# Performance work log

Hardware: AMD Instinct MI355X
Metric: run time of the kernel (lower is better)

## Reference

```python
import jax, jax.numpy as jnp
import numpy as np

# dims: S spaces, B batch, T tokens, D = dense_dim = concept_dim, K codebook size
S, B, T, D, K = 8, 8, 2048, 64, 512
BN_EPS = 1e-3  # keras BatchNormalization default


def setup_inputs() -> dict:
    key = jax.random.key(0)
    k0, k1, k2 = jax.random.split(key, 3)
    x = jax.random.normal(k0, (B, T, D), jnp.float32)
    W = jax.random.normal(k1, (S, D, D), jnp.float32) * 0.1   # per-space Dense kernels
    b = jnp.zeros((S, D), jnp.float32)                         # per-space Dense biases
    gamma = jnp.ones((S, D), jnp.float32)                      # BN scale
    beta = jnp.zeros((S, D), jnp.float32)                      # BN shift
    bn_mean = jnp.zeros((S, D), jnp.float32)                   # BN moving mean
    bn_var = jnp.ones((S, D), jnp.float32)                     # BN moving var
    E = jax.random.normal(k2, (S, K, D), jnp.float32)          # per-space codebooks
    return dict(x=x, W=W, b=b, gamma=gamma, beta=beta,
                bn_mean=bn_mean, bn_var=bn_var, E=E)


def reference(x, W, b, gamma, beta, bn_mean, bn_var, E):
    # per-space projection: Dense -> BatchNorm (inference) -> softmax gate
    proj = jnp.einsum('btd,sde->sbte', x, W) + b[:, None, None, :]          # [S,B,T,D]
    inv = jax.lax.rsqrt(bn_var + BN_EPS)
    bn = gamma[:, None, None, :] * (proj - bn_mean[:, None, None, :]) * inv[:, None, None, :] \
         + beta[:, None, None, :]
    att = jax.nn.softmax(bn, axis=-1)
    z = x[None] * att                                                       # z_e_att, [S,B,T,D]

    # squared euclidean distance to each code; argmin(norm) == argmin(dist^2)
    d2 = (jnp.sum(z * z, axis=-1, keepdims=True)
          - 2.0 * jnp.einsum('sbtc,skc->sbtk', z, E)
          + jnp.sum(E * E, axis=-1)[:, None, None, :])                      # [S,B,T,K]
    z_k = jnp.argmin(d2, axis=-1)                                           # [S,B,T] int

    # gather nearest codes per space, then add_n over spaces (set_att != 0)
    z_q_s = E[jnp.arange(S)[:, None, None], z_k]                            # [S,B,T,D]
    z_q = jnp.sum(z_q_s, axis=0)                                            # [B,T,D]
    z_e = jnp.sum(z, axis=0)                                                # [B,T,D]
    z_k = z_k.astype(jnp.int64) if z_k.dtype != jnp.int64 else z_k          # tf.argmin -> int64
    return z_q, z_e, z_k
```

## Files before the change

kernel.cpp:

```cpp
#include <hip/hip_runtime.h>
#include <cfloat>
#include <cmath>

#define SN 8
#define DN 64
#define KN 512
#define NN 16384
#define CK 64
#define REPAIR_THR 2e-3f
#define GAP_IK 8u
#define MAXFLAG 32768

#define WS_CNT 0
#define WS_SCL 16
#define WS_OFF (16 + SN*DN)
#define WS_E2  (WS_OFF + SN*DN)
#define WS_ENT (WS_E2 + SN*KN)
#define WS_WTH (WS_ENT + MAXFLAG)
#define WS_WTL (WS_WTH + SN*64*32)
#define WS_EH  (WS_WTL + SN*64*32)
#define WS_EL  (WS_EH + SN*KN*32)
#define WS_ZP  (WS_EL + SN*KN*32)
#define WS_E2S (WS_ZP + SN*NN*DN)
#define WS_END (WS_E2S + SN*KN)

#define LDS_ZH 0
#define LDS_ZL 8192
#define LDS_E0 16384
#define LDS_TOTAL 49152

#define FB_LDS_R2    17408
#define FB_LDS_TAIL  33792
#define FB_LDS_TOTAL 34816

typedef __attribute__((ext_vector_type(8))) short bf16x8;
typedef __attribute__((ext_vector_type(4))) short s16x4;
typedef __attribute__((ext_vector_type(4))) float f32x4;

__device__ inline short bf_hi(float f, float& rem) {
    unsigned u = __float_as_uint(f);
    unsigned r = (u + 0x7fffu + ((u >> 16) & 1u)) & 0xffff0000u;
    rem = f - __uint_as_float(r);
    return (short)(r >> 16);
}
__device__ inline short bf_rn(float f) {
    unsigned u = __float_as_uint(f);
    return (short)((u + 0x7fffu + ((u >> 16) & 1u)) >> 16);
}
__device__ inline void cvt4(float a, float b, float c, float d, s16x4& h, s16x4& l) {
    float r0, r1, r2, r3;
    h.x = bf_hi(a, r0); h.y = bf_hi(b, r1); h.z = bf_hi(c, r2); h.w = bf_hi(d, r3);
    l.x = bf_rn(r0); l.y = bf_rn(r1); l.z = bf_rn(r2); l.w = bf_rn(r3);
}

union U8 { bf16x8 v; s16x4 q[2]; };

__global__ void prep_all_kernel(const float* __restrict__ b, const float* __restrict__ gamma,
                                const float* __restrict__ beta, const float* __restrict__ bmean,
                                const float* __restrict__ bvar, const float* __restrict__ W,
                                const float* __restrict__ E, float* __restrict__ ws) {
    __shared__ float wt[64][65];
    const int blk = blockIdx.x, tid = threadIdx.x;
    if (blk < 256) {
        int idx = blk * 256 + tid;
        int sk = idx >> 4, c4 = idx & 15;
        int k = sk & (KN - 1);
        float4 g = ((const float4*)E)[(size_t)sk * 16 + c4];
        s16x4 h4, l4;
        cvt4(g.x, g.y, g.z, g.w, h4, l4);
        size_t off = ((size_t)sk * 128 + c4 * 8) ^ ((k & 7) << 4);
        *(s16x4*)((char*)(ws + WS_EH) + off) = h4;
        *(s16x4*)((char*)(ws + WS_EL) + off) = l4;
    } else if (blk < 264) {
        int s = blk - 256;
        #pragma unroll
        for (int r = 0; r < 4; ++r) {
            int i = r * 256 + tid;
            float4 g = ((const float4*)W)[(size_t)s * 1024 + i];
            int d = i >> 4, c4 = i & 15;
            wt[d][c4 * 4 + 0] = g.x; wt[d][c4 * 4 + 1] = g.y;
            wt[d][c4 * 4 + 2] = g.z; wt[d][c4 * 4 + 3] = g.w;
        }
        __syncthreads();
        #pragma unroll
        for (int r = 0; r < 4; ++r) {
            int j = r * 256 + tid;
            int e = j >> 4, c4 = j & 15;
            s16x4 h4, l4;
            cvt4(wt[c4 * 4 + 0][e], wt[c4 * 4 + 1][e], wt[c4 * 4 + 2][e], wt[c4 * 4 + 3][e], h4, l4);
            size_t off = (size_t)(s * 64 + e) * 128 + c4 * 8;
            *(s16x4*)((char*)(ws + WS_WTH) + off) = h4;
            *(s16x4*)((char*)(ws + WS_WTL) + off) = l4;
        }
    } else {
        int t2 = (blk - 264) * 256 + tid;
        if (t2 < SN * KN) {
            const float* er = E + (size_t)t2 * DN;
            double a = 0.0;
            for (int d = 0; d < DN; ++d) { double v = (double)er[d]; a = fma(v, v, a); }
            ws[WS_E2 + t2]  = (float)a;
            ws[WS_E2S + t2] = (float)(a * 4096.0);
        }
        int u = t2 - SN * KN;
        if (u >= 0 && u < SN * DN) {
            double inv = 1.0 / sqrt((double)bvar[u] + 0.001);
            double sc  = (double)gamma[u] * inv;
            ws[WS_SCL + u] = (float)sc;
            ws[WS_OFF + u] = (float)(((double)b[u] - (double)bmean[u]) * sc + (double)beta[u]);
        }
    }
}

__global__ void prep_kernel(const float* __restrict__ b, const float* __restrict__ gamma,
                            const float* __restrict__ beta, const float* __restrict__ bmean,
                            const float* __restrict__ bvar, const float* __restrict__ E,
                            float* __restrict__ ws) {
    int tid = blockIdx.x * 256 + threadIdx.x;
    if (tid < SN * KN) {
        const float* er = E + (size_t)tid * DN;
        double a = 0.0;
        for (int d = 0; d < DN; ++d) { double v = (double)er[d]; a = fma(v, v, a); }
        ws[WS_E2 + tid] = (float)a;
    }
    int u = tid - SN * KN;
    if (u >= 0 && u < SN * DN) {
        double inv = 1.0 / sqrt((double)bvar[u] + 0.001);
        double sc  = (double)gamma[u] * inv;
        ws[WS_SCL + u] = (float)sc;
        ws[WS_OFF + u] = (float)(((double)b[u] - (double)bmean[u]) * sc + (double)beta[u]);
    }
}

__launch_bounds__(256, 3)
__global__ void main_kernel(const float* __restrict__ x, float* __restrict__ ws,
                            float* __restrict__ out, int entcap) {
    extern __shared__ char smraw[];
    const int tid = threadIdx.x;
    const int s  = blockIdx.y;
    const int n0 = blockIdx.x * 64;
    const int lane = tid & 63;
    const int w    = tid >> 6;
    const int cc   = lane & 15;
    const int kq   = lane >> 4;
    const int arow = w * 16 + cc;
    const int axor = (arow & 7) << 4;

    const char* eimg_h = (const char*)(ws + WS_EH) + (size_t)s * KN * 128;
    const char* eimg_l = (const char*)(ws + WS_EL) + (size_t)s * KN * 128;

    float4 pf0 = *(const float4*)(eimg_h + tid * 16);
    float4 pf1 = *(const float4*)(eimg_h + 4096 + tid * 16);
    float4 pf2 = *(const float4*)(eimg_l + tid * 16);
    float4 pf3 = *(const float4*)(eimg_l + 4096 + tid * 16);

    U8 xah[2], xal[2];
    #pragma unroll
    for (int ks = 0; ks < 2; ++ks) {
        const float* xr = x + (size_t)(n0 + arow) * DN + ks * 32 + kq * 8;
        float4 a = *(const float4*)xr;
        float4 b2 = *(const float4*)(xr + 4);
        s16x4 h0, l0, h1, l1;
        cvt4(a.x, a.y, a.z, a.w, h0, l0);
        cvt4(b2.x, b2.y, b2.z, b2.w, h1, l1);
        xah[ks].q[0] = h0; xah[ks].q[1] = h1;
        xal[ks].q[0] = l0; xal[ks].q[1] = l1;
    }

    const char* wimg_h = (const char*)(ws + WS_WTH) + (size_t)s * 64 * 128;
    const char* wimg_l = (const char*)(ws + WS_WTL) + (size_t)s * 64 * 128;
    f32x4 pa[4];
    #pragma unroll
    for (int nt = 0; nt < 4; ++nt) pa[nt] = (f32x4){0.f, 0.f, 0.f, 0.f};
    #pragma unroll
    for (int ks = 0; ks < 2; ++ks) {
        #pragma unroll
        for (int nt = 0; nt < 4; ++nt) {
            int brow = nt * 16 + cc;
            bf16x8 bh = *(const bf16x8*)(wimg_h + brow * 128 + ks * 64 + kq * 16);
            bf16x8 bl = *(const bf16x8*)(wimg_l + brow * 128 + ks * 64 + kq * 16);
            pa[nt] = __builtin_amdgcn_mfma_f32_16x16x32_bf16(xah[ks].v, bh, pa[nt], 0, 0, 0);
            pa[nt] = __builtin_amdgcn_mfma_f32_16x16x32_bf16(xah[ks].v, bl, pa[nt], 0, 0, 0);
            pa[nt] = __builtin_amdgcn_mfma_f32_16x16x32_bf16(xal[ks].v, bh, pa[nt], 0, 0, 0);
        }
    }

    float sclv[4], oflv[4];
    #pragma unroll
    for (int nt = 0; nt < 4; ++nt) {
        sclv[nt] = ws[WS_SCL + s * 64 + nt * 16 + cc];
        oflv[nt] = ws[WS_OFF + s * 64 + nt * 16 + cc];
    }
    float zzq[4];
    #pragma unroll
    for (int r = 0; r < 4; ++r) {
        int t = w * 16 + kq * 4 + r;
        float v0 = fmaf(pa[0][r], sclv[0], oflv[0]);
        float v1 = fmaf(pa[1][r], sclv[1], oflv[1]);
        float v2 = fmaf(pa[2][r], sclv[2], oflv[2]);
        float v3 = fmaf(pa[3][r], sclv[3], oflv[3]);
        float mx = fmaxf(fmaxf(v0, v1), fmaxf(v2, v3));
        mx = fmaxf(mx, __shfl_xor(mx, 1)); mx = fmaxf(mx, __shfl_xor(mx, 2));
        mx = fmaxf(mx, __shfl_xor(mx, 4)); mx = fmaxf(mx, __shfl_xor(mx, 8));
        float e0 = __expf(v0 - mx), e1 = __expf(v1 - mx);
        float e2v = __expf(v2 - mx), e3 = __expf(v3 - mx);
        float sm = e0 + e1 + e2v + e3;
        sm += __shfl_xor(sm, 1); sm += __shfl_xor(sm, 2);
        sm += __shfl_xor(sm, 4); sm += __shfl_xor(sm, 8);
        float inv = 1.0f / sm;
        float att[4] = { e0 * inv, e1 * inv, e2v * inv, e3 * inv };
        float zz = 0.f;
        int txor = (t & 7) << 4;
        #pragma unroll
        for (int nt = 0; nt < 4; ++nt) {
            int e = nt * 16 + cc;
            float xv = x[(size_t)(n0 + t) * DN + e];
            float z = xv * att[nt];
            zz += z * z;
            float rem; short zh = bf_hi(z, rem); short zl = bf_rn(rem);
            int zoff = (t * 128 + e * 2) ^ txor;
            *(short*)(smraw + LDS_ZH + zoff) = zh;
            *(short*)(smraw + LDS_ZL + zoff) = zl;
            ws[WS_ZP + ((size_t)s * NN + n0 + t) * DN + e] = z;
        }
        zz += __shfl_xor(zz, 1); zz += __shfl_xor(zz, 2);
        zz += __shfl_xor(zz, 4); zz += __shfl_xor(zz, 8);
        zzq[r] = (zz + 16.f) * 4096.f;
    }

    bf16x8 zah[2], zal[2];
    #pragma unroll
    for (int ks = 0; ks < 2; ++ks) {
        int aoff = (arow * 128 + kq * 16 + ks * 64) ^ axor;
        zah[ks] = *(const bf16x8*)(smraw + LDS_ZH + aoff);
        zal[ks] = *(const bf16x8*)(smraw + LDS_ZL + aoff);
    }

    unsigned m1[4], m2[4];
    #pragma unroll
    for (int r = 0; r < 4; ++r) { m1[r] = 0xFFFFFFFFu; m2[r] = 0xFFFFFFFFu; }

    int p = 0;
    #pragma unroll 1
    for (int c = 0; c < KN / CK; ++c) {
        char* ebuf = smraw + LDS_E0 + p * 16384;
        *(float4*)(ebuf + tid * 16) = pf0;
        *(float4*)(ebuf + 4096 + tid * 16) = pf1;
        *(float4*)(ebuf + 8192 + tid * 16) = pf2;
        *(float4*)(ebuf + 12288 + tid * 16) = pf3;
        __syncthreads();

        int kk = c * CK;
        if (c < KN / CK - 1) {
            const char* nbh = eimg_h + (size_t)(kk + CK) * 128;
            const char* nbl = eimg_l + (size_t)(kk + CK) * 128;
            pf0 = *(const float4*)(nbh + tid * 16);
            pf1 = *(const float4*)(nbh + 4096 + tid * 16);
            pf2 = *(const float4*)(nbl + tid * 16);
            pf3 = *(const float4*)(nbl + 4096 + tid * 16);
        }
        float e2v[4];
        #pragma unroll
        for (int nt = 0; nt < 4; ++nt) e2v[nt] = ws[WS_E2S + s * KN + kk + nt * 16 + cc];

        f32x4 acc[4];
        #pragma unroll
        for (int nt = 0; nt < 4; ++nt) acc[nt] = (f32x4){0.f, 0.f, 0.f, 0.f};
        #pragma unroll
        for (int ks = 0; ks < 2; ++ks) {
            #pragma unroll
            for (int nt = 0; nt < 4; ++nt) {
                int brow = nt * 16 + cc;
                int boff = (brow * 128 + kq * 16 + ks * 64) ^ ((brow & 7) << 4);
                bf16x8 bh = *(const bf16x8*)(ebuf + boff);
                bf16x8 bl = *(const bf16x8*)(ebuf + 8192 + boff);
                acc[nt] = __builtin_amdgcn_mfma_f32_16x16x32_bf16(zah[ks], bh, acc[nt], 0, 0, 0);
                acc[nt] = __builtin_amdgcn_mfma_f32_16x16x32_bf16(zah[ks], bl, acc[nt], 0, 0, 0);
                acc[nt] = __builtin_amdgcn_mfma_f32_16x16x32_bf16(zal[ks], bh, acc[nt], 0, 0, 0);
            }
        }
        #pragma unroll
        for (int nt = 0; nt < 4; ++nt) {
            unsigned kx = (unsigned)(kk + nt * 16 + cc);
            #pragma unroll
            for (int r = 0; r < 4; ++r) {
                float cell = fmaf(-8192.f, acc[nt][r], zzq[r] + e2v[nt]);
                unsigned key = (((unsigned)cell) << 9) | kx;
                m2[r] = min(m2[r], max(m1[r], key));
                m1[r] = min(m1[r], key);
            }
        }
        p ^= 1;
    }

    #pragma unroll
    for (int mask = 1; mask <= 8; mask <<= 1) {
        #pragma unroll
        for (int r = 0; r < 4; ++r) {
            unsigned o1 = (unsigned)__shfl_xor((int)m1[r], mask);
            unsigned o2 = (unsigned)__shfl_xor((int)m2[r], mask);
            unsigned hi = max(m1[r], o1);
            m1[r] = min(m1[r], o1);
            m2[r] = min(min(m2[r], o2), hi);
        }
    }
    #pragma unroll
    for (int r = 0; r < 4; ++r) {
        int n = n0 + w * 16 + kq * 4 + r;
        if (cc == 0) {
            int k1 = (int)(m1[r] & 511u);
            out[2 * NN * DN + s * NN + n] = (float)k1;
            if ((m2[r] >> 9) - (m1[r] >> 9) <= GAP_IK) {
                int idx = atomicAdd((int*)ws, 1);
                if (idx < entcap) ((int*)ws)[WS_ENT + idx] = (s << 14) | n;
            }
        }
    }
}

__launch_bounds__(256, 4)
__global__ void main_fb_kernel(const float* __restrict__ x, const float* __restrict__ W,
                               const float* __restrict__ E, float* __restrict__ ws,
                               float* __restrict__ out, int entcap) {
    extern __shared__ char smraw[];
    float4* xs4 = (float4*)smraw;
    float4* ws4 = (float4*)(smraw + FB_LDS_R2);
    char* ehb = smraw;
    char* elb = smraw + 8192;
    char* zhb = smraw + FB_LDS_R2;
    char* zlb = smraw + FB_LDS_R2 + 8192;
    float* tailf = (float*)(smraw + FB_LDS_TAIL);
    float* e2s = tailf; float* scl = tailf + 64; float* ofl = tailf + 128; float* zzs = tailf + 192;

    const int tid = threadIdx.x;
    const int tg = tid >> 4, lg = tid & 15;
    const int s  = blockIdx.y;
    const int n0 = blockIdx.x * 64;
    const float4* xg4 = (const float4*)x;
    const float4* Wg4 = (const float4*)W;
    const float4* Eg4 = (const float4*)E;

    #pragma unroll
    for (int r = 0; r < 4; ++r) {
        int i = r * 256 + tid;
        xs4[(i >> 4) * 17 + (i & 15)] = xg4[n0 * 16 + i];
        ws4[i] = Wg4[s * 1024 + i];
    }
    if (tid < 64) { scl[tid] = ws[WS_SCL + s * 64 + tid]; ofl[tid] = ws[WS_OFF + s * 64 + tid]; }
    __syncthreads();

    float pa[4][4];
    #pragma unroll
    for (int ti = 0; ti < 4; ++ti)
        #pragma unroll
        for (int j = 0; j < 4; ++j) pa[ti][j] = 0.f;
    #pragma unroll 4
    for (int c = 0; c < 16; ++c) {
        float4 xv[4], wv[4];
        #pragma unroll
        for (int ti = 0; ti < 4; ++ti) xv[ti] = xs4[(tg * 4 + ti) * 17 + c];
        #pragma unroll
        for (int dd = 0; dd < 4; ++dd) wv[dd] = ws4[(c * 4 + dd) * 16 + lg];
        #pragma unroll
        for (int ti = 0; ti < 4; ++ti) {
            float a0 = pa[ti][0], a1 = pa[ti][1], a2 = pa[ti][2], a3 = pa[ti][3];
            a0 = fmaf(xv[ti].x, wv[0].x, a0); a0 = fmaf(xv[ti].y, wv[1].x, a0);
            a0 = fmaf(xv[ti].z, wv[2].x, a0); a0 = fmaf(xv[ti].w, wv[3].x, a0);
            a1 = fmaf(xv[ti].x, wv[0].y, a1); a1 = fmaf(xv[ti].y, wv[1].y, a1);
            a1 = fmaf(xv[ti].z, wv[2].y, a1); a1 = fmaf(xv[ti].w, wv[3].y, a1);
            a2 = fmaf(xv[ti].x, wv[0].z, a2); a2 = fmaf(xv[ti].y, wv[1].z, a2);
            a2 = fmaf(xv[ti].z, wv[2].z, a2); a2 = fmaf(xv[ti].w, wv[3].z, a2);
            a3 = fmaf(xv[ti].x, wv[0].w, a3); a3 = fmaf(xv[ti].y, wv[1].w, a3);
            a3 = fmaf(xv[ti].z, wv[2].w, a3); a3 = fmaf(xv[ti].w, wv[3].w, a3);
            pa[ti][0] = a0; pa[ti][1] = a1; pa[ti][2] = a2; pa[ti][3] = a3;
        }
    }
    __syncthreads();

    {
        float s0 = scl[lg * 4 + 0], s1 = scl[lg * 4 + 1], s2 = scl[lg * 4 + 2], s3 = scl[lg * 4 + 3];
        float o0 = ofl[lg * 4 + 0], o1 = ofl[lg * 4 + 1], o2 = ofl[lg * 4 + 2], o3 = ofl[lg * 4 + 3];
        #pragma unroll
        for (int ti = 0; ti < 4; ++ti) {
            int t = tg * 4 + ti;
            float v0 = fmaf(pa[ti][0], s0, o0);
            float v1 = fmaf(pa[ti][1], s1, o1);
            float v2 = fmaf(pa[ti][2], s2, o2);
            float v3 = fmaf(pa[ti][3], s3, o3);
            float mx = fmaxf(fmaxf(v0, v1), fmaxf(v2, v3));
            mx = fmaxf(mx, __shfl_xor(mx, 1)); mx = fmaxf(mx, __shfl_xor(mx, 2));
            mx = fmaxf(mx, __shfl_xor(mx, 4)); mx = fmaxf(mx, __shfl_xor(mx, 8));
            float e0 = expf(v0 - mx), e1 = expf(v1 - mx), e2v = expf(v2 - mx), e3 = expf(v3 - mx);
            float sm = e0 + e1 + e2v + e3;
            sm += __shfl_xor(sm, 1); sm += __shfl_xor(sm, 2);
            sm += __shfl_xor(sm, 4); sm += __shfl_xor(sm, 8);
            float inv = 1.0f / sm;
            float4 xv = xs4[t * 17 + lg];
            float z0 = xv.x * (e0 * inv), z1 = xv.y * (e1 * inv);
            float z2 = xv.z * (e2v * inv), z3 = xv.w * (e3 * inv);
            float zz = z0 * z0 + z1 * z1 + z2 * z2 + z3 * z3;
            zz += __shfl_xor(zz, 1); zz += __shfl_xor(zz, 2);
            zz += __shfl_xor(zz, 4); zz += __shfl_xor(zz, 8);
            if (lg == 0) zzs[t] = zz;
            s16x4 h4, l4;
            cvt4(z0, z1, z2, z3, h4, l4);
            int zoff = (t * 128 + lg * 8) ^ ((t & 7) << 4);
            *(s16x4*)(zhb + zoff) = h4;
            *(s16x4*)(zlb + zoff) = l4;
            float* pz = out + NN * DN + (size_t)(n0 + t) * DN + lg * 4;
            atomicAdd(pz + 0, z0); atomicAdd(pz + 1, z1);
            atomicAdd(pz + 2, z2); atomicAdd(pz + 3, z3);
        }
    }
    __syncthreads();

    const int lane = tid & 63;
    const int w    = tid >> 6;
    const int arow = w * 16 + (lane & 15);
    const int kg16 = (lane >> 4) * 16;
    const int axor = (arow & 7) << 4;
    const int abase = arow * 128 + kg16;

    float zzv[4];
    #pragma unroll
    for (int r = 0; r < 4; ++r) zzv[r] = zzs[w * 16 + (lane >> 4) * 4 + r];

    float m1[4], m2[4]; int k1[4];
    #pragma unroll
    for (int r = 0; r < 4; ++r) { m1[r] = FLT_MAX; m2[r] = FLT_MAX; k1[r] = 0x7fffffff; }

    for (int kk = 0; kk < KN; kk += CK) {
        __syncthreads();
        #pragma unroll
        for (int r = 0; r < 4; ++r) {
            int i = r * 256 + tid;
            float4 g = Eg4[(s * KN + kk) * 16 + i];
            int row = i >> 4, c4 = i & 15;
            s16x4 h4, l4;
            cvt4(g.x, g.y, g.z, g.w, h4, l4);
            int off = (row * 128 + c4 * 8) ^ ((row & 7) << 4);
            *(s16x4*)(ehb + off) = h4;
            *(s16x4*)(elb + off) = l4;
        }
        if (tid < 64) e2s[tid] = ws[WS_E2 + s * KN + kk + tid];
        __syncthreads();

        f32x4 acc[4];
        #pragma unroll
        for (int nt = 0; nt < 4; ++nt) acc[nt] = (f32x4){0.f, 0.f, 0.f, 0.f};
        #pragma unroll
        for (int ks = 0; ks < 2; ++ks) {
            int aoff = (abase + ks * 64) ^ axor;
            bf16x8 ah = *(const bf16x8*)(zhb + aoff);
            bf16x8 al = *(const bf16x8*)(zlb + aoff);
            #pragma unroll
            for (int nt = 0; nt < 4; ++nt) {
                int brow = nt * 16 + (lane & 15);
                int boff = (brow * 128 + kg16 + ks * 64) ^ ((brow & 7) << 4);
                bf16x8 bh = *(const bf16x8*)(ehb + boff);
                bf16x8 bl = *(const bf16x8*)(elb + boff);
                acc[nt] = __builtin_amdgcn_mfma_f32_16x16x32_bf16(ah, bh, acc[nt], 0, 0, 0);
                acc[nt] = __builtin_amdgcn_mfma_f32_16x16x32_bf16(ah, bl, acc[nt], 0, 0, 0);
                acc[nt] = __builtin_amdgcn_mfma_f32_16x16x32_bf16(al, bh, acc[nt], 0, 0, 0);
            }
        }
        #pragma unroll
        for (int nt = 0; nt < 4; ++nt) {
            float e2v = e2s[nt * 16 + (lane & 15)];
            int kx = kk + nt * 16 + (lane & 15);
            #pragma unroll
            for (int r = 0; r < 4; ++r) {
                float d2 = fmaf(-2.0f, acc[nt][r], zzv[r]) + e2v;
                if (d2 < m1[r]) { m2[r] = m1[r]; m1[r] = d2; k1[r] = kx; }
                else if (d2 < m2[r]) { m2[r] = d2; }
            }
        }
    }

    #pragma unroll
    for (int mask = 1; mask <= 8; mask <<= 1) {
        #pragma unroll
        for (int r = 0; r < 4; ++r) {
            float om1 = __shfl_xor(m1[r], mask);
            int   ok1 = __shfl_xor(k1[r], mask);
            float om2 = __shfl_xor(m2[r], mask);
            bool better = (om1 < m1[r]) || (om1 == m1[r] && ok1 < k1[r]);
            float nm2 = better ? fminf(m1[r], om2) : fminf(om1, m2[r]);
            if (better) { m1[r] = om1; k1[r] = ok1; }
            m2[r] = nm2;
        }
    }
    #pragma unroll
    for (int r = 0; r < 4; ++r) {
        int t = w * 16 + (lane >> 4) * 4 + r;
        int n = n0 + t;
        if ((lane & 15) == 0) {
            out[2 * NN * DN + s * NN + n] = (float)k1[r];
            if (m2[r] - m1[r] < REPAIR_THR) {
                int idx = atomicAdd((int*)ws, 1);
                if (idx < entcap) ((int*)ws)[WS_ENT + idx] = (s << 14) | n;
            }
        }
        int kb = __shfl(k1[r], lane & 48);
        float4 eg = Eg4[(s * KN + kb) * 16 + (lane & 15)];
        float* q = out + (size_t)n * DN + (lane & 15) * 4;
        atomicAdd(q + 0, eg.x); atomicAdd(q + 1, eg.y);
        atomicAdd(q + 2, eg.z); atomicAdd(q + 3, eg.w);
    }
}

__global__ void reduce_kernel(const float* __restrict__ E, const float* __restrict__ ws,
                              float* __restrict__ out) {
    int idx = blockIdx.x * 256 + threadIdx.x;
    int n = idx >> 4, c = idx & 15;
    const float4* zp4 = (const float4*)(ws + WS_ZP);
    float4 ze = make_float4(0.f, 0.f, 0.f, 0.f);
    #pragma unroll
    for (int s = 0; s < SN; ++s) {
        float4 v = zp4[((size_t)s * NN + n) * 16 + c];
        ze.x += v.x; ze.y += v.y; ze.z += v.z; ze.w += v.w;
    }
    ((float4*)out)[NN * 16 + (size_t)n * 16 + c] = ze;

    float4 zq = make_float4(0.f, 0.f, 0.f, 0.f);
    #pragma unroll
    for (int s = 0; s < SN; ++s) {
        int k = (int)(out[2 * NN * DN + s * NN + n] + 0.5f);
        float4 e = ((const float4*)E)[((size_t)s * KN + k) * 16 + c];
        zq.x += e.x; zq.y += e.y; zq.z += e.z; zq.w += e.w;
    }
    ((float4*)out)[(size_t)n * 16 + c] = zq;
}

__global__ void repair_kernel(const float* __restrict__ x, const float* __restrict__ W,
                              const float* __restrict__ b, const float* __restrict__ gamma,
                              const float* __restrict__ beta, const float* __restrict__ bmean,
                              const float* __restrict__ bvar, const float* __restrict__ E,
                              float* __restrict__ ws, float* __restrict__ out, int entcap) {
    __shared__ double zd[64];
    __shared__ double red[256];
    __shared__ int redk[256];
    __shared__ double zzsh;
    __shared__ int shk[2];
    int cnt = ((int*)ws)[0]; if (cnt > entcap) cnt = entcap;
    const int tid = threadIdx.x;
    for (int idx = blockIdx.x; idx < cnt; idx += gridDim.x) {
        int code = ((int*)ws)[WS_ENT + idx];
        int s = code >> 14, n = code & (NN - 1);
        int e = tid & 63, q = tid >> 6;
        const float* xrow = x + (size_t)n * 64;
        double p0 = 0.0, p1 = 0.0, p2 = 0.0, p3 = 0.0;
        for (int d = q * 16; d < q * 16 + 16; d += 4) {
            p0 = fma((double)xrow[d],     (double)W[((size_t)s * 64 + d) * 64 + e],     p0);
            p1 = fma((double)xrow[d + 1], (double)W[((size_t)s * 64 + d + 1) * 64 + e], p1);
            p2 = fma((double)xrow[d + 2], (double)W[((size_t)s * 64 + d + 2) * 64 + e], p2);
            p3 = fma((double)xrow[d + 3], (double)W[((size_t)s * 64 + d + 3) * 64 + e], p3);
        }
        red[tid] = (p0 + p1) + (p2 + p3);
        __syncthreads();
        if (tid < 64) {
            double proj = (red[tid] + red[tid + 64]) + (red[tid + 128] + red[tid + 192]);
            double inv = 1.0 / sqrt((double)bvar[s * 64 + e] + 0.001);
            double bn = (double)gamma[s * 64 + e] * ((proj + (double)b[s * 64 + e]) - (double)bmean[s * 64 + e]) * inv
                      + (double)beta[s * 64 + e];
            double m = bn;
            #pragma unroll
            for (int mask = 1; mask <= 32; mask <<= 1) m = fmax(m, __shfl_xor(m, mask));
            double ex = exp(bn - m);
            double sm = ex;
            #pragma unroll
            for (int mask = 1; mask <= 32; mask <<= 1) sm += __shfl_xor(sm, mask);
            double z = (double)xrow[e] * (ex / sm);
            zd[e] = z;
            double zz = z * z;
            #pragma unroll
            for (int mask = 1; mask <= 32; mask <<= 1) zz += __shfl_xor(zz, mask);
            if (tid == 0) zzsh = zz;
        }
        __syncthreads();
        double bv = DBL_MAX; int bk = 1 << 30;
        for (int k = tid; k < KN; k += 256) {
            const float* er = E + ((size_t)s * KN + k) * 64;
            double d0 = 0.0, d1 = 0.0, d2a = 0.0, d3 = 0.0;
            double f0 = 0.0, f1 = 0.0, f2 = 0.0, f3 = 0.0;
            for (int d = 0; d < 64; d += 4) {
                double e0 = (double)er[d], e1 = (double)er[d + 1];
                double e2d = (double)er[d + 2], e3d = (double)er[d + 3];
                d0 = fma(zd[d], e0, d0);     d1 = fma(zd[d + 1], e1, d1);
                d2a = fma(zd[d + 2], e2d, d2a); d3 = fma(zd[d + 3], e3d, d3);
                f0 = fma(e0, e0, f0); f1 = fma(e1, e1, f1);
                f2 = fma(e2d, e2d, f2); f3 = fma(e3d, e3d, f3);
            }
            double dot = (d0 + d1) + (d2a + d3);
            double e2t = (f0 + f1) + (f2 + f3);
            double d2v = (zzsh - 2.0 * dot) + e2t;
            if (d2v < bv) { bv = d2v; bk = k; }
        }
        #pragma unroll
        for (int mask = 1; mask <= 32; mask <<= 1) {
            double ov = __shfl_xor(bv, mask);
            int   ok = __shfl_xor(bk, mask);
            if (ov < bv || (ov == bv && ok < bk)) { bv = ov; bk = ok; }
        }
        if ((tid & 63) == 0) { red[tid >> 6] = bv; redk[tid >> 6] = bk; }
        __syncthreads();
        if (tid == 0) {
            double m = red[0]; int mk = redk[0];
            for (int i = 1; i < 4; ++i)
                if (red[i] < m || (red[i] == m && redk[i] < mk)) { m = red[i]; mk = redk[i]; }
            int kold = (int)(out[2 * NN * 64 + s * NN + n] + 0.5f);
            shk[0] = mk; shk[1] = kold;
            out[2 * NN * 64 + s * NN + n] = (float)mk;
        }
        __syncthreads();
        int mk = shk[0], kold = shk[1];
        if (mk != kold && tid < 64)
            atomicAdd(out + n * 64 + tid, E[((size_t)s * KN + mk) * 64 + tid] - E[((size_t)s * KN + kold) * 64 + tid]);
        __syncthreads();
    }
}

extern "C" void kernel_launch(void* const* d_in, const int* in_sizes, int n_in,
                              void* d_out, int out_size, void* d_ws, size_t ws_size,
                              hipStream_t stream) {
    const float* x     = (const float*)d_in[0];
    const float* W     = (const float*)d_in[1];
    const float* b     = (const float*)d_in[2];
    const float* gamma = (const float*)d_in[3];
    const float* beta  = (const float*)d_in[4];
    const float* bmean = (const float*)d_in[5];
    const float* bvar  = (const float*)d_in[6];
    const float* E     = (const float*)d_in[7];
    float* out = (float*)d_out;
    float* ws  = (float*)d_ws;

    bool staged = ws_size >= (size_t)WS_END * 4;

    long avail = (long)(ws_size / 4) - WS_ENT - 16;
    if (avail < 0) avail = 0;
    int entcap = (int)(avail > MAXFLAG ? MAXFLAG : avail);
    if (staged) entcap = MAXFLAG;

    hipMemsetAsync(d_ws, 0, 64, stream);
    dim3 grid(256, 8);
    if (staged) {
        prep_all_kernel<<<282, 256, 0, stream>>>(b, gamma, beta, bmean, bvar, W, E, ws);
        main_kernel<<<grid, 256, LDS_TOTAL, stream>>>(x, ws, out, entcap);
        reduce_kernel<<<1024, 256, 0, stream>>>(E, ws, out);
    } else {
        prep_kernel<<<18, 256, 0, stream>>>(b, gamma, beta, bmean, bvar, E, ws);
        hipMemsetAsync(d_out, 0, (size_t)(2 * NN * DN) * sizeof(float), stream);
        main_fb_kernel<<<grid, 256, FB_LDS_TOTAL, stream>>>(x, W, E, ws, out, entcap);
    }
    repair_kernel<<<2048, 256, 0, stream>>>(x, W, b, gamma, beta, bmean, bvar, E, ws, out, entcap);
}
```

Baseline: 153.0 us.

## Double block tile to 128 rows, restage codebook pipeline, coalesce z spill

Main kernel blocks grow from 256 to 512 threads and cover 128 tokens each, so every codebook chunk staged in LDS is reused by twice as many rows. The codebook prefetch is restructured so each chunk is written to the alternate buffer after the compute, giving one barrier per chunk. The per-element z spill to workspace is replaced by a coalesced float4 write reconstructed from the bf16 hi/lo pair held in LDS. The workspace memset is folded into the prep kernel, and the repair gap threshold is halved. Risks: the reconstructed z is not bit-identical to the fp32 value, and the larger LDS footprint and block size can lower occupancy.

```diff
diff --git a/kernel.cpp b/kernel.cpp
--- a/kernel.cpp
+++ b/kernel.cpp
@@ -8,7 +8,7 @@
 #define NN 16384
 #define CK 64
 #define REPAIR_THR 2e-3f
-#define GAP_IK 8u
+#define GAP_IK 4u
 #define MAXFLAG 32768
 
 #define WS_CNT 0
@@ -25,9 +25,9 @@
 #define WS_END (WS_E2S + SN*KN)
 
 #define LDS_ZH 0
-#define LDS_ZL 8192
-#define LDS_E0 16384
-#define LDS_TOTAL 49152
+#define LDS_ZL 16384
+#define LDS_E0 32768
+#define LDS_TOTAL 65536
 
 #define FB_LDS_R2    17408
 #define FB_LDS_TAIL  33792
@@ -51,6 +51,9 @@
     float r0, r1, r2, r3;
     h.x = bf_hi(a, r0); h.y = bf_hi(b, r1); h.z = bf_hi(c, r2); h.w = bf_hi(d, r3);
     l.x = bf_rn(r0); l.y = bf_rn(r1); l.z = bf_rn(r2); l.w = bf_rn(r3);
+}
+__device__ inline float bf2f(unsigned short h) {
+    return __uint_as_float(((unsigned)h) << 16);
 }
 
 union U8 { bf16x8 v; s16x4 q[2]; };
@@ -93,6 +96,7 @@
             *(s16x4*)((char*)(ws + WS_WTL) + off) = l4;
         }
     } else {
+        if (blk == 264 && tid < 16) ((int*)ws)[tid] = 0;
         int t2 = (blk - 264) * 256 + tid;
         if (t2 < SN * KN) {
             const float* er = E + (size_t)t2 * DN;
@@ -131,13 +135,13 @@
     }
 }
 
-__launch_bounds__(256, 3)
+__launch_bounds__(512, 4)
 __global__ void main_kernel(const float* __restrict__ x, float* __restrict__ ws,
                             float* __restrict__ out, int entcap) {
     extern __shared__ char smraw[];
     const int tid = threadIdx.x;
     const int s  = blockIdx.y;
-    const int n0 = blockIdx.x * 64;
+    const int n0 = blockIdx.x * 128;
     const int lane = tid & 63;
     const int w    = tid >> 6;
     const int cc   = lane & 15;
@@ -149,9 +153,7 @@
     const char* eimg_l = (const char*)(ws + WS_EL) + (size_t)s * KN * 128;
 
     float4 pf0 = *(const float4*)(eimg_h + tid * 16);
-    float4 pf1 = *(const float4*)(eimg_h + 4096 + tid * 16);
-    float4 pf2 = *(const float4*)(eimg_l + tid * 16);
-    float4 pf3 = *(const float4*)(eimg_l + 4096 + tid * 16);
+    float4 pf1 = *(const float4*)(eimg_l + tid * 16);
 
     U8 xah[2], xal[2];
     #pragma unroll
@@ -220,7 +222,6 @@
             int zoff = (t * 128 + e * 2) ^ txor;
             *(short*)(smraw + LDS_ZH + zoff) = zh;
             *(short*)(smraw + LDS_ZL + zoff) = zl;
-            ws[WS_ZP + ((size_t)s * NN + n0 + t) * DN + e] = z;
         }
         zz += __shfl_xor(zz, 1); zz += __shfl_xor(zz, 2);
         zz += __shfl_xor(zz, 4); zz += __shfl_xor(zz, 8);
@@ -235,6 +236,28 @@
         zal[ks] = *(const bf16x8*)(smraw + LDS_ZL + aoff);
     }
 
+    {
+        char* eb = smraw + LDS_E0;
+        *(float4*)(eb + tid * 16) = pf0;
+        *(float4*)(eb + 8192 + tid * 16) = pf1;
+    }
+    __syncthreads();
+
+    #pragma unroll
+    for (int j = 0; j < 4; ++j) {
+        int a = tid + j * 512;
+        int t = a >> 4, q = a & 15;
+        int off = (t * 128 + q * 8) ^ ((t & 7) << 4);
+        s16x4 h = *(const s16x4*)(smraw + LDS_ZH + off);
+        s16x4 l = *(const s16x4*)(smraw + LDS_ZL + off);
+        float4 zv;
+        zv.x = bf2f((unsigned short)h.x) + bf2f((unsigned short)l.x);
+        zv.y = bf2f((unsigned short)h.y) + bf2f((unsigned short)l.y);
+        zv.z = bf2f((unsigned short)h.z) + bf2f((unsigned short)l.z);
+        zv.w = bf2f((unsigned short)h.w) + bf2f((unsigned short)l.w);
+        ((float4*)(ws + WS_ZP))[((size_t)s * NN + n0 + t) * 16 + q] = zv;
+    }
+
     unsigned m1[4], m2[4];
     #pragma unroll
     for (int r = 0; r < 4; ++r) { m1[r] = 0xFFFFFFFFu; m2[r] = 0xFFFFFFFFu; }
@@ -242,21 +265,11 @@
     int p = 0;
     #pragma unroll 1
     for (int c = 0; c < KN / CK; ++c) {
-        char* ebuf = smraw + LDS_E0 + p * 16384;
-        *(float4*)(ebuf + tid * 16) = pf0;
-        *(float4*)(ebuf + 4096 + tid * 16) = pf1;
-        *(float4*)(ebuf + 8192 + tid * 16) = pf2;
-        *(float4*)(ebuf + 12288 + tid * 16) = pf3;
-        __syncthreads();
-
+        const char* ebuf = smraw + LDS_E0 + p * 16384;
         int kk = c * CK;
         if (c < KN / CK - 1) {
-            const char* nbh = eimg_h + (size_t)(kk + CK) * 128;
-            const char* nbl = eimg_l + (size_t)(kk + CK) * 128;
-            pf0 = *(const float4*)(nbh + tid * 16);
-            pf1 = *(const float4*)(nbh + 4096 + tid * 16);
-            pf2 = *(const float4*)(nbl + tid * 16);
-            pf3 = *(const float4*)(nbl + 4096 + tid * 16);
+            pf0 = *(const float4*)(eimg_h + (size_t)(kk + CK) * 128 + tid * 16);
+            pf1 = *(const float4*)(eimg_l + (size_t)(kk + CK) * 128 + tid * 16);
         }
         float e2v[4];
         #pragma unroll
@@ -289,7 +302,13 @@
                 m1[r] = min(m1[r], key);
             }
         }
-        p ^= 1;
+        if (c < KN / CK - 1) {
+            char* nb = smraw + LDS_E0 + (p ^ 1) * 16384;
+            *(float4*)(nb + tid * 16) = pf0;
+            *(float4*)(nb + 8192 + tid * 16) = pf1;
+            __syncthreads();
+            p ^= 1;
+        }
     }
 
     #pragma unroll
@@ -640,15 +659,17 @@
     int entcap = (int)(avail > MAXFLAG ? MAXFLAG : avail);
     if (staged) entcap = MAXFLAG;
 
-    hipMemsetAsync(d_ws, 0, 64, stream);
-    dim3 grid(256, 8);
     if (staged) {
+        hipFuncSetAttribute((const void*)main_kernel, hipFuncAttributeMaxDynamicSharedMemorySize, LDS_TOTAL);
         prep_all_kernel<<<282, 256, 0, stream>>>(b, gamma, beta, bmean, bvar, W, E, ws);
-        main_kernel<<<grid, 256, LDS_TOTAL, stream>>>(x, ws, out, entcap);
+        dim3 grid(128, 8);
+        main_kernel<<<grid, 512, LDS_TOTAL, stream>>>(x, ws, out, entcap);
         reduce_kernel<<<1024, 256, 0, stream>>>(E, ws, out);
     } else {
+        hipMemsetAsync(d_ws, 0, 64, stream);
         prep_kernel<<<18, 256, 0, stream>>>(b, gamma, beta, bmean, bvar, E, ws);
         hipMemsetAsync(d_out, 0, (size_t)(2 * NN * DN) * sizeof(float), stream);
+        dim3 grid(256, 8);
         main_fb_kernel<<<grid, 256, FB_LDS_TOTAL, stream>>>(x, W, E, ws, out, entcap);
     }
     repair_kernel<<<2048, 256, 0, stream>>>(x, W, b, gamma, beta, bmean, bvar, E, ws, out, entcap);
```

Measured after the change: 150.3 us. About the same (-1.7%).
